# Kernel optimization log

Measured on AMD Instinct MI355X. Metric: run time of the kernel, lower is better.

The kernel has to match this reference:

```python
import jax, jax.numpy as jnp
import numpy as np

N_LAYER = 4; D_MODEL = 512; D_INNER = 1024; D_STATE = 16
DT_RANK = 32; D_CONV = 3; VOCAB = 128; SEQ = 1024; HID = 2048; BATCH = 4
EPS = 1e-5

def layernorm(x, w, b):
    m = jnp.mean(x, -1, keepdims=True)
    v = jnp.mean((x - m) ** 2, -1, keepdims=True)
    return (x - m) * jax.lax.rsqrt(v + EPS) * w + b

def rmsnorm(x, w):
    return x * jax.lax.rsqrt(jnp.mean(x * x, -1, keepdims=True) + EPS) * w

def selective_scan(u, delta, A, B, C, D):
    # u, delta: (b,l,d); B,C: (b,l,n); A: (d,n); D: (d,)
    def step(s, inp):
        d_t, B_t, C_t, u_t = inp  # (b,d),(b,n),(b,n),(b,d)
        dA = jnp.exp(d_t[..., None] * A)                    # (b,d,n)
        dBu = (d_t * u_t)[..., None] * B_t[:, None, :]      # (b,d,n)
        s = dA * s + dBu
        return s, jnp.einsum('bdn,bn->bd', s, C_t)
    b, l, d = u.shape
    s0 = jnp.zeros((b, d, A.shape[1]), u.dtype)
    xs = (delta.swapaxes(0, 1), B.swapaxes(0, 1), C.swapaxes(0, 1), u.swapaxes(0, 1))
    _, ys = jax.lax.scan(step, s0, xs)
    return ys.swapaxes(0, 1) + u * D

def mamba_block(x, ln_w, ln_b, W_in, cw, cb, W_x, W_dt, b_dt, A_log, Dp, W_out):
    # ResidualBlock in source is norm -> mixer with NO residual add
    x = layernorm(x, ln_w, ln_b)
    xr = x @ W_in                               # (b,l,2*d_inner)
    xs, res = jnp.split(xr, 2, axis=-1)
    # depthwise causal conv (torch pads d_conv-1 both sides then slices [:l] == left-pad only)
    xc = jax.lax.conv_general_dilated(
        xs.swapaxes(1, 2), cw[:, None, :], (1,), [(D_CONV - 1, 0)],
        feature_group_count=D_INNER, dimension_numbers=('NCH', 'OIH', 'NCH'))
    xc = jax.nn.silu((xc + cb[:, None]).swapaxes(1, 2))  # (b,l,d_inner)
    A = -jnp.exp(A_log)
    x_dbl = xc @ W_x
    delta, B, C = jnp.split(x_dbl, [DT_RANK, DT_RANK + D_STATE], axis=-1)
    delta = jax.nn.softplus(delta @ W_dt + b_dt)
    y = selective_scan(xc, delta, A, B, C, Dp)
    return (y * jax.nn.silu(res)) @ W_out

def reference(inp, W_emb, b_emb,
              ln1_w, ln1_b, Win1, cw1, cb1, Wx1, Wdt1, bdt1, Alog1, D1, Wout1,
              ln2_w, ln2_b, Win2, cw2, cb2, Wx2, Wdt2, bdt2, Alog2, D2, Wout2,
              lnl_w, lnl_b, Wl1, bl1, Wl2, bl2,
              normf_w, normf_b, W_head, b_head):
    x = inp @ W_emb + b_emb
    x1 = x; x2 = x
    for i in range(N_LAYER):
        x1 = mamba_block(x1, ln1_w[i], ln1_b[i], Win1[i], cw1[i], cb1[i],
                         Wx1[i], Wdt1[i], bdt1[i], Alog1[i], D1[i], Wout1[i])
        x2 = mamba_block(jnp.flip(x2, 1), ln2_w[i], ln2_b[i], Win2[i], cw2[i], cb2[i],
                         Wx2[i], Wdt2[i], bdt2[i], Alog2[i], D2[i], Wout2[i])
        x = x1 + jnp.flip(x2, 1) + x
        xp = x.swapaxes(1, 2)                   # (b, d_model, seq)
        h = layernorm(xp, lnl_w[i], lnl_b[i]) if i == 0 else rmsnorm(xp, lnl_w[i])
        h = jax.nn.relu(h @ Wl1[i] + bl1[i]) @ Wl2[i] + bl2[i]
        x = h.swapaxes(1, 2) + x
        x1 = x; x2 = x
    x = layernorm(x, normf_w, normf_b)
    return x @ W_head + b_head

def setup_inputs():
    key = jax.random.key(0)
    ks = iter(jax.random.split(key, 80))
    r = lambda shape, s=0.02: jax.random.normal(next(ks), shape, jnp.float32) * s
    L, D, DI, N, R, K, V, S, H = N_LAYER, D_MODEL, D_INNER, D_STATE, DT_RANK, D_CONV, VOCAB, SEQ, HID
    def dirp():
        return [jnp.ones((L, D)), jnp.zeros((L, D)), r((L, D, 2 * DI)),
                r((L, DI, K), 0.2), jnp.zeros((L, DI)), r((L, DI, R + 2 * N)),
                r((L, R, DI), 0.1), jnp.zeros((L, DI)),
                jnp.broadcast_to(jnp.log(jnp.arange(1.0, N + 1)), (L, DI, N)) + 0.0,
                jnp.ones((L, DI)), r((L, DI, D))]
    p1 = dirp(); p2 = dirp()
    d = {"inp": jax.random.normal(next(ks), (BATCH, S, V), jnp.float32),
         "W_emb": r((V, D)), "b_emb": jnp.zeros((D,))}
    n1 = ["ln1_w", "ln1_b", "Win1", "cw1", "cb1", "Wx1", "Wdt1", "bdt1", "Alog1", "D1", "Wout1"]
    n2 = ["ln2_w", "ln2_b", "Win2", "cw2", "cb2", "Wx2", "Wdt2", "bdt2", "Alog2", "D2", "Wout2"]
    d.update(dict(zip(n1, p1))); d.update(dict(zip(n2, p2)))
    d.update({"lnl_w": jnp.ones((L, S)), "lnl_b": jnp.zeros((L, S)),
              "Wl1": r((L, S, H)), "bl1": jnp.zeros((L, H)),
              "Wl2": r((L, H, S)), "bl2": jnp.zeros((L, S)),
              "normf_w": jnp.ones((D,)), "normf_b": jnp.zeros((D,)),
              "W_head": r((D, V)), "b_head": jnp.zeros((V,))})
    return d
```

## Files before the change

kernel.cpp:

```cpp
#include <hip/hip_runtime.h>
#include <math.h>

#define NLAYER 4
#define DM 512
#define DI 1024
#define NS 16
#define RK 32
#define VOC 128
#define S 1024
#define HD 2048
#define B 4
#define TOK (B*S)
#define TOK2 (2*TOK)
#define EPSF 1e-5f
#define NC 32
#define CL 32

typedef unsigned short u16;
typedef __attribute__((ext_vector_type(8))) short bf16x8;
typedef __attribute__((ext_vector_type(4))) float f32x4;

__device__ __forceinline__ float siluf(float x){ return x / (1.f + __expf(-x)); }
__device__ __forceinline__ float softplusf(float x){
    return x > 20.f ? x : __logf(1.f + __expf(x));
}
__device__ __forceinline__ u16 f2bf(float f){
    unsigned u = __float_as_uint(f);
    u += 0x7fffu + ((u >> 16) & 1u);
    return (u16)(u >> 16);
}
__device__ __forceinline__ float bf2f(u16 v){ return __uint_as_float(((unsigned)v) << 16); }

__device__ __forceinline__ void powchain16(float a1, float* e){
    float a2 = a1*a1, a4 = a2*a2, a8 = a4*a4;
    e[0]=a1;      e[1]=a2;      e[2]=a2*a1;   e[3]=a4;
    e[4]=a4*a1;   e[5]=a4*a2;   e[6]=a4*e[2]; e[7]=a8;
    e[8]=a8*a1;   e[9]=a8*a2;   e[10]=a8*e[2];e[11]=a8*a4;
    e[12]=a8*e[4];e[13]=a8*e[5];e[14]=a8*e[6];e[15]=a8*a8;
}

template<int BM, int ACT, bool BIAS, bool OUTBF16>
__launch_bounds__(256)
__global__ void mgemm_k(const u16* __restrict__ A,
                        const u16* __restrict__ Bt0, const u16* __restrict__ Bt1,
                        const float* __restrict__ bias0, const float* __restrict__ bias1,
                        void* __restrict__ Cv, int M, int N, int K, int Ksl, int mh,
                        size_t zstride)
{
    constexpr int LOGBM = (BM == 128) ? 7 : 6;
    constexpr int NI = (BM == 128) ? 4 : 2;
    constexpr int SSZ = BM*32 + 128*32;
    __shared__ u16 smem[3*SSZ];
    const int tid  = threadIdx.x;
    const int wave = tid >> 6;
    const int lane = tid & 63;
    const int nwg  = gridDim.x * gridDim.y;
    const int orig = blockIdx.y * gridDim.x + blockIdx.x;
    const int q = nwg >> 3, r = nwg & 7;
    const int xcd = orig & 7, sid = orig >> 3;
    const int nid = (xcd < r ? xcd*(q+1) : r*(q+1) + (xcd-r)*q) + sid;
    const int m_blk = (nid / gridDim.x) * BM;
    const int n_blk = (nid % gridDim.x) * 128;
    const int dir = (m_blk >= mh) ? 1 : 0;
    const u16* Bt = dir ? Bt1 : Bt0;
    const float* bias = dir ? bias1 : bias0;
    const int wm = (BM == 128) ? (wave & 1) * 64 : 0;
    const int wn = (BM == 128) ? (wave >> 1) * 64 : wave * 32;
    const int kbeg = blockIdx.z * Ksl;

    f32x4 acc[4][NI];
    #pragma unroll
    for (int i=0;i<4;i++)
        #pragma unroll
        for (int j=0;j<NI;j++){ f32x4 z = {0.f,0.f,0.f,0.f}; acc[i][j] = z; }

    const u16* Ag = A + (size_t)(m_blk + (tid & (BM-1))) * K + ((tid >> LOGBM) * 8) + kbeg;
    const u16* Bg = Bt + (size_t)(n_blk + (tid & 127)) * K + ((tid >> 7) * 8) + kbeg;
    const int la = lane & 15, ga = lane >> 4;

    auto stage = [&](int k0, int st){
        u16* Al = smem + st*SSZ;
        u16* Bl = Al + BM*32;
        #pragma unroll
        for (int c = 0; c < BM/64; ++c)
            __builtin_amdgcn_global_load_lds(
                (const __attribute__((address_space(1))) unsigned int*)(Ag + k0 + c*16),
                (__attribute__((address_space(3))) unsigned int*)&Al[(c*256 + tid)*8],
                16, 0, 0);
        #pragma unroll
        for (int c = 0; c < 2; ++c)
            __builtin_amdgcn_global_load_lds(
                (const __attribute__((address_space(1))) unsigned int*)(Bg + k0 + c*16),
                (__attribute__((address_space(3))) unsigned int*)&Bl[(c*256 + tid)*8],
                16, 0, 0);
    };

    const int niter = Ksl >> 5;
    stage(0, 0);
    stage(32, 1);
    for (int it = 0; it < niter; ++it) {
        if (it < niter-1) {
            if (BM == 128)
                asm volatile("s_waitcnt vmcnt(4) lgkmcnt(0)\n\ts_barrier" ::: "memory");
            else
                asm volatile("s_waitcnt vmcnt(3) lgkmcnt(0)\n\ts_barrier" ::: "memory");
        } else {
            asm volatile("s_waitcnt vmcnt(0) lgkmcnt(0)\n\ts_barrier" ::: "memory");
        }
        if (it + 2 < niter) stage((it+2)*32, (it+2)%3);
        const u16* Ab = smem + (it%3)*SSZ;
        const u16* Bb = Ab + BM*32;
        bf16x8 af[4], bf[NI];
        #pragma unroll
        for (int mi=0;mi<4;mi++)
            af[mi] = *(const bf16x8*)&Ab[((ga*BM) + wm + mi*16 + la)*8];
        #pragma unroll
        for (int ni=0;ni<NI;ni++)
            bf[ni] = *(const bf16x8*)&Bb[((ga*128) + wn + ni*16 + la)*8];
        #pragma unroll
        for (int mi=0;mi<4;mi++)
            #pragma unroll
            for (int ni=0;ni<NI;ni++)
                acc[mi][ni] = __builtin_amdgcn_mfma_f32_16x16x32_bf16(af[mi], bf[ni], acc[mi][ni], 0,0,0);
    }

    const int col = lane & 15;
    const int r4  = (lane >> 4) * 4;
    asm volatile("s_waitcnt lgkmcnt(0)\n\ts_barrier" ::: "memory");
    if (OUTBF16) {
        u16* Cs = smem;
        #pragma unroll
        for (int mi=0;mi<4;mi++){
            #pragma unroll
            for (int ni=0;ni<NI;ni++){
                int cc = wn + ni*16 + col;
                float bv = BIAS ? bias[n_blk + cc] : 0.f;
                #pragma unroll
                for (int r=0;r<4;r++){
                    float v = acc[mi][ni][r] + bv;
                    if (ACT==1) v = fmaxf(v, 0.f);
                    Cs[(wm + mi*16 + r4 + r)*128 + cc] = f2bf(v);
                }
            }
        }
        asm volatile("s_waitcnt lgkmcnt(0)\n\ts_barrier" ::: "memory");
        u16* Cg = (u16*)Cv + (size_t)blockIdx.z * zstride;
        #pragma unroll
        for (int k=0;k<BM/16;k++){
            int q2 = k*256 + tid;
            int row = q2 >> 4, co = (q2 & 15) * 8;
            uint4 v = *(const uint4*)&Cs[row*128 + co];
            *(uint4*)(Cg + (size_t)(m_blk+row)*N + n_blk + co) = v;
        }
    } else {
        float* Csf = (float*)smem;
        float* Cg = (float*)Cv + (size_t)blockIdx.z * zstride;
        #pragma unroll
        for (int h=0; h<2; ++h){
            if ((wn >> 6) == h){
                #pragma unroll
                for (int mi=0;mi<4;mi++){
                    #pragma unroll
                    for (int ni=0;ni<NI;ni++){
                        int cc = wn - h*64 + ni*16 + col;
                        float bv = BIAS ? bias[n_blk + h*64 + cc] : 0.f;
                        #pragma unroll
                        for (int r=0;r<4;r++){
                            float v = acc[mi][ni][r] + bv;
                            if (ACT==1) v = fmaxf(v, 0.f);
                            Csf[(mi*16 + r4 + r)*64 + cc] = v;
                        }
                    }
                }
            }
            asm volatile("s_waitcnt lgkmcnt(0)\n\ts_barrier" ::: "memory");
            #pragma unroll
            for (int k=0;k<4;k++){
                int q2 = k*256 + tid;
                int row = q2 >> 4, co = (q2 & 15) * 4;
                float4 v = *(const float4*)&Csf[row*64 + co];
                *(float4*)(Cg + (size_t)(m_blk+row)*N + n_blk + h*64 + co) = v;
            }
            if (h == 0)
                asm volatile("s_waitcnt lgkmcnt(0)\n\ts_barrier" ::: "memory");
        }
    }
}

__launch_bounds__(256)
__global__ void gemm_wx_k(const u16* __restrict__ A, const u16* __restrict__ Bt,
                          float* __restrict__ C, int K, int Ksl)
{
    constexpr int SSZ = 128*32 + 128*32;
    __shared__ u16 smem[3*SSZ];
    const int tid  = threadIdx.x;
    const int wave = tid >> 6;
    const int lane = tid & 63;
    const int m_blk = blockIdx.y * 128;
    const int dir = (m_blk >= TOK) ? 1 : 0;
    const int wm = (wave & 1) * 64;
    const int wn = (wave >> 1) * 64;
    const int kbeg = blockIdx.z * Ksl;

    f32x4 acc[4][4];
    #pragma unroll
    for (int i=0;i<4;i++)
        #pragma unroll
        for (int j=0;j<4;j++){ f32x4 z = {0.f,0.f,0.f,0.f}; acc[i][j] = z; }

    const u16* Ag = A + (size_t)(m_blk + (tid & 127)) * K + ((tid >> 7) * 8) + kbeg;
    const u16* Bg = Bt + (size_t)(tid & 127) * K + ((tid >> 7) * 8) + kbeg;
    const int la = lane & 15, ga = lane >> 4;

    auto stage = [&](int k0, int st){
        u16* Al = smem + st*SSZ;
        u16* Bl = Al + 128*32;
        #pragma unroll
        for (int c = 0; c < 2; ++c){
            __builtin_amdgcn_global_load_lds(
                (const __attribute__((address_space(1))) unsigned int*)(Ag + k0 + c*16),
                (__attribute__((address_space(3))) unsigned int*)&Al[(c*256 + tid)*8],
                16, 0, 0);
            __builtin_amdgcn_global_load_lds(
                (const __attribute__((address_space(1))) unsigned int*)(Bg + k0 + c*16),
                (__attribute__((address_space(3))) unsigned int*)&Bl[(c*256 + tid)*8],
                16, 0, 0);
        }
    };

    const int niter = Ksl >> 5;
    stage(0, 0);
    stage(32, 1);
    for (int it = 0; it < niter; ++it) {
        if (it < niter-1)
            asm volatile("s_waitcnt vmcnt(4) lgkmcnt(0)\n\ts_barrier" ::: "memory");
        else
            asm volatile("s_waitcnt vmcnt(0) lgkmcnt(0)\n\ts_barrier" ::: "memory");
        if (it + 2 < niter) stage((it+2)*32, (it+2)%3);
        const u16* Ab = smem + (it%3)*SSZ;
        const u16* Bb = Ab + 128*32;
        bf16x8 af[4], bf[4];
        #pragma unroll
        for (int mi=0;mi<4;mi++)
            af[mi] = *(const bf16x8*)&Ab[((ga*128) + wm + mi*16 + la)*8];
        #pragma unroll
        for (int ni=0;ni<4;ni++)
            bf[ni] = *(const bf16x8*)&Bb[((ga*128) + wn + ni*16 + la)*8];
        #pragma unroll
        for (int mi=0;mi<4;mi++)
            #pragma unroll
            for (int ni=0;ni<4;ni++)
                acc[mi][ni] = __builtin_amdgcn_mfma_f32_16x16x32_bf16(af[mi], bf[ni], acc[mi][ni], 0,0,0);
    }

    const int col = lane & 15;
    const int r4  = (lane >> 4) * 4;
    #pragma unroll
    for (int mi=0;mi<4;mi++){
        #pragma unroll
        for (int ni=0;ni<4;ni++){
            int cg = wn + ni*16 + col;
            if ((cg >> 6) != dir) continue;
            int co = cg & 63;
            #pragma unroll
            for (int r=0;r<4;r++){
                int rg = m_blk + wm + mi*16 + r4 + r;
                atomicAdd(C + (size_t)rg*64 + co, acc[mi][ni][r]);
            }
        }
    }
}

__global__ void wtconv2_k(const float* __restrict__ W0, const float* __restrict__ W1,
                          u16* __restrict__ T0, u16* __restrict__ T1, int K, int N)
{
    const float* W = blockIdx.z ? W1 : W0;
    u16* Wt = blockIdx.z ? T1 : T0;
    __shared__ float tile[32][33];
    int n0 = blockIdx.x*32, k0 = blockIdx.y*32;
    int tx = threadIdx.x, ty = threadIdx.y;
    #pragma unroll
    for (int j=0;j<32;j+=8)
        tile[ty+j][tx] = W[(size_t)(k0+ty+j)*N + n0+tx];
    __syncthreads();
    #pragma unroll
    for (int j=0;j<32;j+=8)
        Wt[(size_t)(n0+ty+j)*K + k0+tx] = f2bf(tile[tx][ty+j]);
}

template<int ACT, bool BIAS>
__launch_bounds__(256)
__global__ void gemm_k(const float* __restrict__ A, int lda,
                       const float* __restrict__ Bm, int ldb,
                       const float* __restrict__ bias,
                       float* __restrict__ C, int ldc, int K)
{
    __shared__ float As[16][64];
    __shared__ float Bs[16][64];
    const int tid = threadIdx.x;
    const int n0 = blockIdx.x * 64;
    const int m0 = blockIdx.y * 64;
    const int tn = (tid & 15) * 4;
    const int tm = (tid >> 4) * 4;
    const int am = tid >> 2;
    const int ak = (tid & 3) * 4;
    const int bk = tid >> 4;
    const int bn = (tid & 15) * 4;
    float acc[4][4] = {};
    for (int k0 = 0; k0 < K; k0 += 16) {
        float4 av = *(const float4*)(A + (size_t)(m0 + am) * lda + k0 + ak);
        float4 bv = *(const float4*)(Bm + (size_t)(k0 + bk) * ldb + n0 + bn);
        __syncthreads();
        As[ak+0][am] = av.x; As[ak+1][am] = av.y; As[ak+2][am] = av.z; As[ak+3][am] = av.w;
        *(float4*)(&Bs[bk][bn]) = bv;
        __syncthreads();
        #pragma unroll
        for (int k = 0; k < 16; ++k) {
            float4 a = *(const float4*)(&As[k][tm]);
            float4 b = *(const float4*)(&Bs[k][tn]);
            float aa[4] = {a.x,a.y,a.z,a.w};
            float bb[4] = {b.x,b.y,b.z,b.w};
            #pragma unroll
            for (int i=0;i<4;i++)
                #pragma unroll
                for (int j=0;j<4;j++)
                    acc[i][j] = fmaf(aa[i], bb[j], acc[i][j]);
        }
    }
    #pragma unroll
    for (int i=0;i<4;i++)
        #pragma unroll
        for (int j=0;j<4;j++){
            float v = acc[i][j];
            if (BIAS) v += bias[n0+tn+j];
            if (ACT==1) v = fmaxf(v, 0.f);
            C[(size_t)(m0+tm+i)*ldc + n0+tn+j] = v;
        }
}

__launch_bounds__(256)
__global__ void gemm_sk_k(const float* __restrict__ A, int lda,
                          const float* __restrict__ Bm, int ldb,
                          const float* __restrict__ bias,
                          float* __restrict__ C, int ldc, int kslice)
{
    __shared__ float As[16][64];
    __shared__ float Bs[16][64];
    const int tid = threadIdx.x;
    const int n0 = blockIdx.x * 64;
    const int m0 = blockIdx.y * 64;
    const int kbeg = blockIdx.z * kslice;
    const int tn = (tid & 15) * 4;
    const int tm = (tid >> 4) * 4;
    const int am = tid >> 2;
    const int ak = (tid & 3) * 4;
    const int bk = tid >> 4;
    const int bn = (tid & 15) * 4;
    float acc[4][4] = {};
    for (int k0 = kbeg; k0 < kbeg + kslice; k0 += 16) {
        float4 av = *(const float4*)(A + (size_t)(m0 + am) * lda + k0 + ak);
        float4 bv = *(const float4*)(Bm + (size_t)(k0 + bk) * ldb + n0 + bn);
        __syncthreads();
        As[ak+0][am] = av.x; As[ak+1][am] = av.y; As[ak+2][am] = av.z; As[ak+3][am] = av.w;
        *(float4*)(&Bs[bk][bn]) = bv;
        __syncthreads();
        #pragma unroll
        for (int k = 0; k < 16; ++k) {
            float4 a = *(const float4*)(&As[k][tm]);
            float4 b = *(const float4*)(&Bs[k][tn]);
            float aa[4] = {a.x,a.y,a.z,a.w};
            float bb[4] = {b.x,b.y,b.z,b.w};
            #pragma unroll
            for (int i=0;i<4;i++)
                #pragma unroll
                for (int j=0;j<4;j++)
                    acc[i][j] = fmaf(aa[i], bb[j], acc[i][j]);
        }
    }
    #pragma unroll
    for (int i=0;i<4;i++)
        #pragma unroll
        for (int j=0;j<4;j++){
            float v = acc[i][j];
            if (bias && blockIdx.z == 0) v += bias[n0+tn+j];
            atomicAdd(C + (size_t)(m0+tm+i)*ldc + n0+tn+j, v);
        }
}

__launch_bounds__(256)
__global__ void gemm_dt_k(const float* __restrict__ xdbl,
                          const float* __restrict__ Wdt0, const float* __restrict__ Wdt1,
                          const float* __restrict__ bdt0, const float* __restrict__ bdt1,
                          u16* __restrict__ delta)
{
    __shared__ float As[32][64];
    __shared__ float Bs[32][64];
    const int tid = threadIdx.x;
    const int n0 = blockIdx.x * 64;
    const int m0 = blockIdx.y * 64;
    const int dir = (m0 >= TOK) ? 1 : 0;
    const float* Wdt = dir ? Wdt1 : Wdt0;
    const float* bdt = dir ? bdt1 : bdt0;
    const int am = tid >> 2;
    const int ak = (tid & 3) * 8;
    {
        float4 a0 = *(const float4*)(xdbl + (size_t)(m0 + am) * 64 + ak);
        float4 a1 = *(const float4*)(xdbl + (size_t)(m0 + am) * 64 + ak + 4);
        As[ak+0][am]=a0.x; As[ak+1][am]=a0.y; As[ak+2][am]=a0.z; As[ak+3][am]=a0.w;
        As[ak+4][am]=a1.x; As[ak+5][am]=a1.y; As[ak+6][am]=a1.z; As[ak+7][am]=a1.w;
        int bk = tid >> 4;
        int bn = (tid & 15) * 4;
        *(float4*)(&Bs[bk][bn])    = *(const float4*)(Wdt + (size_t)bk*DI + n0 + bn);
        *(float4*)(&Bs[bk+16][bn]) = *(const float4*)(Wdt + (size_t)(bk+16)*DI + n0 + bn);
    }
    __syncthreads();
    const int tn = (tid & 15) * 4;
    const int tm = (tid >> 4) * 4;
    float acc[4][4] = {};
    #pragma unroll
    for (int k = 0; k < 32; ++k) {
        float4 a = *(const float4*)(&As[k][tm]);
        float4 b = *(const float4*)(&Bs[k][tn]);
        float aa[4] = {a.x,a.y,a.z,a.w};
        float bb[4] = {b.x,b.y,b.z,b.w};
        #pragma unroll
        for (int i=0;i<4;i++)
            #pragma unroll
            for (int j=0;j<4;j++)
                acc[i][j] = fmaf(aa[i], bb[j], acc[i][j]);
    }
    #pragma unroll
    for (int i=0;i<4;i++)
        #pragma unroll
        for (int j=0;j<4;j++)
            delta[(size_t)(m0+tm+i)*DI + n0+tn+j] = f2bf(softplusf(acc[i][j] + bdt[n0+tn+j]));
}

template<int LEN, bool RMS, bool OB>
__launch_bounds__(256)
__global__ void norm_k(const float* __restrict__ in, const float* __restrict__ w,
                       const float* __restrict__ b, void* __restrict__ outv)
{
    constexpr int PER = LEN/256;
    const int row = blockIdx.x;
    const float* x = in + (size_t)row * LEN;
    float v[PER];
    float s = 0.f, ss = 0.f;
    #pragma unroll
    for (int i=0;i<PER;i++){ v[i] = x[threadIdx.x + i*256]; s += v[i]; ss += v[i]*v[i]; }
    #pragma unroll
    for (int off=32; off; off>>=1){ s += __shfl_down(s, off); ss += __shfl_down(ss, off); }
    __shared__ float sh[8];
    int wid = threadIdx.x >> 6;
    if ((threadIdx.x & 63) == 0){ sh[wid] = s; sh[wid+4] = ss; }
    __syncthreads();
    s = sh[0]+sh[1]+sh[2]+sh[3]; ss = sh[4]+sh[5]+sh[6]+sh[7];
    float mean = RMS ? 0.f : s / (float)LEN;
    float var  = ss / (float)LEN - mean*mean;
    float r = rsqrtf(var + EPSF);
    #pragma unroll
    for (int i=0;i<PER;i++){
        int c = threadIdx.x + i*256;
        float y = (v[i]-mean)*r*w[c];
        if (!RMS) y += b[c];
        if (OB) ((u16*)outv)[(size_t)row*LEN + c] = f2bf(y);
        else    ((float*)outv)[(size_t)row*LEN + c] = y;
    }
}

__launch_bounds__(256)
__global__ void norm2_k(const float* __restrict__ in,
                        const float* __restrict__ w0, const float* __restrict__ b0,
                        const float* __restrict__ w1, const float* __restrict__ b1,
                        u16* __restrict__ outv)
{
    const int row = blockIdx.x;
    const int t = row & (TOK-1);
    const float* w = (row >= TOK) ? w1 : w0;
    const float* b = (row >= TOK) ? b1 : b0;
    const float* x = in + (size_t)t * DM;
    float v[2];
    float s = 0.f, ss = 0.f;
    #pragma unroll
    for (int i=0;i<2;i++){ v[i] = x[threadIdx.x + i*256]; s += v[i]; ss += v[i]*v[i]; }
    #pragma unroll
    for (int off=32; off; off>>=1){ s += __shfl_down(s, off); ss += __shfl_down(ss, off); }
    __shared__ float sh[8];
    int wid = threadIdx.x >> 6;
    if ((threadIdx.x & 63) == 0){ sh[wid] = s; sh[wid+4] = ss; }
    __syncthreads();
    s = sh[0]+sh[1]+sh[2]+sh[3]; ss = sh[4]+sh[5]+sh[6]+sh[7];
    float mean = s / (float)DM;
    float var  = ss / (float)DM - mean*mean;
    float r = rsqrtf(var + EPSF);
    #pragma unroll
    for (int i=0;i<2;i++){
        int c = threadIdx.x + i*256;
        outv[(size_t)row*DM + c] = f2bf((v[i]-mean)*r*w[c] + b[c]);
    }
}

__launch_bounds__(256)
__global__ void conv_silu2_k(const u16* __restrict__ xr,
                             const float* __restrict__ cw0, const float* __restrict__ cb0,
                             const float* __restrict__ cw1, const float* __restrict__ cb1,
                             u16* __restrict__ xcout)
{
    int idx = blockIdx.x*256 + threadIdx.x;
    int ch = idx & (DI-1);
    int row = idx >> 10;
    int l  = row & (S-1);
    int dir = row >> 12;
    int rev = dir;
    const float* cw = dir ? cw1 : cw0;
    const float* cb = dir ? cb1 : cb0;
    float acc = cb[ch];
    #pragma unroll
    for (int k=0;k<3;k++){
        int lp = rev ? (l + 2 - k) : (l - 2 + k);
        if (lp >= 0 && lp < S)
            acc = fmaf(cw[ch*3+k], bf2f(xr[(size_t)(row - l + lp)*2048 + ch]), acc);
    }
    xcout[(size_t)row*DI + ch] = f2bf(siluf(acc));
}

__launch_bounds__(256)
__global__ void add3_k(const float* __restrict__ xin, const float* __restrict__ yw,
                       float* __restrict__ acc)
{
    int i = (blockIdx.x*256 + threadIdx.x)*4;
    float4 a = *(const float4*)(xin + i);
    float4 b = *(const float4*)(yw + i);
    float4 c = *(const float4*)(yw + (size_t)TOK*DM + i);
    float4 o = {a.x+b.x+c.x, a.y+b.y+c.y, a.z+b.z+c.z, a.w+b.w+c.w};
    *(float4*)(acc + i) = o;
}

__launch_bounds__(256)
__global__ void scan_part1_k(const u16* __restrict__ xc, const u16* __restrict__ delta,
                             const float* __restrict__ xdbl,
                             const float* __restrict__ Alog0, const float* __restrict__ Alog1,
                             float* __restrict__ sumP, float* __restrict__ sumS)
{
    const int g = blockIdx.x;
    const int chg = g & 3;
    const int c   = (g >> 2) & (NC-1);
    const int db  = g >> 7;
    const int dir = db >> 2;
    const int rev = dir;
    const int tid = threadIdx.x;
    const int ch  = chg*256 + tid;

    __shared__ float Bsh[CL][16];
    #pragma unroll
    for (int r=0;r<2;r++){
        int idx = r*256 + tid;
        int j = idx >> 4, w = idx & 15;
        int p = c*CL + j;
        int t = rev ? (S-1-p) : p;
        Bsh[j][w] = xdbl[((size_t)(db*S + t))*64 + 32 + w];
    }
    __syncthreads();

    const float* Alog = dir ? Alog1 : Alog0;
    const float An0 = -__expf(Alog[(size_t)ch*16]);

    float s[16];
    #pragma unroll
    for (int n=0;n<16;n++) s[n] = 0.f;
    float dsum = 0.f;
    for (int j=0;j<CL;j++){
        int p = c*CL + j;
        int t = rev ? (S-1-p) : p;
        size_t tt = (size_t)(db*S + t);
        float dl = bf2f(delta[tt*DI + ch]);
        float ul = bf2f(xc[tt*DI + ch]);
        dsum += dl;
        float dlu = dl*ul;
        float Bv[16];
        *(float4*)&Bv[0]  = *(const float4*)&Bsh[j][0];
        *(float4*)&Bv[4]  = *(const float4*)&Bsh[j][4];
        *(float4*)&Bv[8]  = *(const float4*)&Bsh[j][8];
        *(float4*)&Bv[12] = *(const float4*)&Bsh[j][12];
        float e[16];
        powchain16(__expf(dl*An0), e);
        #pragma unroll
        for (int n=0;n<16;n++)
            s[n] = fmaf(e[n], s[n], dlu*Bv[n]);
    }
    size_t base = ((size_t)(db*NC + c)*DI + ch)*16;
    float P[16];
    powchain16(__expf(dsum*An0), P);
    #pragma unroll
    for (int q=0;q<4;q++){
        *(float4*)(sumP + base + q*4) = *(float4*)&P[q*4];
        *(float4*)(sumS + base + q*4) = *(float4*)&s[q*4];
    }
}

__launch_bounds__(256)
__global__ void scan_part2_k(float* __restrict__ sumP, const float* __restrict__ sumS)
{
    int g = blockIdx.x*256 + threadIdx.x;
    int idx = g & (DI*16 - 1);
    int db = g >> 14;
    float carry = 0.f;
    #pragma unroll 8
    for (int c=0;c<NC;c++){
        size_t o = (size_t)(db*NC + c)*DI*16 + idx;
        float P = sumP[o], Sv = sumS[o];
        sumP[o] = carry;
        carry = fmaf(P, carry, Sv);
    }
}

__launch_bounds__(256)
__global__ void scan_part3_k(const u16* __restrict__ xc, const u16* __restrict__ delta,
                             const float* __restrict__ xdbl,
                             const float* __restrict__ Alog0, const float* __restrict__ Alog1,
                             const float* __restrict__ Dp0, const float* __restrict__ Dp1,
                             const u16* __restrict__ xr, const float* __restrict__ sumI,
                             u16* __restrict__ ybb)
{
    const int g = blockIdx.x;
    const int chg = g & 3;
    const int c   = (g >> 2) & (NC-1);
    const int db  = g >> 7;
    const int dir = db >> 2;
    const int rev = dir;
    const int tid = threadIdx.x;
    const int ch  = chg*256 + tid;

    __shared__ float BC[CL][32];
    #pragma unroll
    for (int r=0;r<4;r++){
        int idx = r*256 + tid;
        int j = idx >> 5, w = idx & 31;
        int p = c*CL + j;
        int t = rev ? (S-1-p) : p;
        BC[j][w] = xdbl[((size_t)(db*S + t))*64 + 32 + w];
    }
    __syncthreads();

    const float* Alog = dir ? Alog1 : Alog0;
    const float An0 = -__expf(Alog[(size_t)ch*16]);
    const float dch = (dir ? Dp1 : Dp0)[ch];

    float s[16];
    size_t base = ((size_t)(db*NC + c)*DI + ch)*16;
    #pragma unroll
    for (int q=0;q<4;q++){
        float4 iv = *(const float4*)(sumI + base + q*4);
        s[q*4+0]=iv.x; s[q*4+1]=iv.y; s[q*4+2]=iv.z; s[q*4+3]=iv.w;
    }
    for (int j=0;j<CL;j++){
        int p = c*CL + j;
        int t = rev ? (S-1-p) : p;
        size_t tt = (size_t)(db*S + t);
        float dl = bf2f(delta[tt*DI + ch]);
        float ul = bf2f(xc[tt*DI + ch]);
        float res = bf2f(xr[tt*2048 + 1024 + ch]);
        float dlu = dl*ul;
        float Bv[16], Cv[16];
        *(float4*)&Bv[0]  = *(const float4*)&BC[j][0];
        *(float4*)&Bv[4]  = *(const float4*)&BC[j][4];
        *(float4*)&Bv[8]  = *(const float4*)&BC[j][8];
        *(float4*)&Bv[12] = *(const float4*)&BC[j][12];
        *(float4*)&Cv[0]  = *(const float4*)&BC[j][16];
        *(float4*)&Cv[4]  = *(const float4*)&BC[j][20];
        *(float4*)&Cv[8]  = *(const float4*)&BC[j][24];
        *(float4*)&Cv[12] = *(const float4*)&BC[j][28];
        float e[16];
        powchain16(__expf(dl*An0), e);
        float y = 0.f;
        #pragma unroll
        for (int n=0;n<16;n++){
            s[n] = fmaf(e[n], s[n], dlu*Bv[n]);
            y = fmaf(s[n], Cv[n], y);
        }
        y = (y + ul*dch) * siluf(res);
        ybb[tt*DI + ch] = f2bf(y);
    }
}

__global__ void transpose_k(const float* __restrict__ in, float* __restrict__ out)
{
    __shared__ float tile[32][33];
    int b = blockIdx.z, s0 = blockIdx.x*32, d0 = blockIdx.y*32;
    int tx = threadIdx.x, ty = threadIdx.y;
    #pragma unroll
    for (int j=0;j<32;j+=8)
        tile[ty+j][tx] = in[((size_t)b*S + s0+ty+j)*DM + d0+tx];
    __syncthreads();
    #pragma unroll
    for (int j=0;j<32;j+=8)
        out[((size_t)b*DM + d0+ty+j)*S + s0+tx] = tile[tx][ty+j];
}
__global__ void transpose_add_k(const float* __restrict__ h, const float* __restrict__ bias,
                                float* __restrict__ x)
{
    __shared__ float tile[32][33];
    int b = blockIdx.z, s0 = blockIdx.x*32, d0 = blockIdx.y*32;
    int tx = threadIdx.x, ty = threadIdx.y;
    #pragma unroll
    for (int j=0;j<32;j+=8){
        size_t o = ((size_t)b*DM + d0+ty+j)*S + s0+tx;
        tile[ty+j][tx] = h[o] + h[o + (size_t)2048*1024];
    }
    __syncthreads();
    #pragma unroll
    for (int j=0;j<32;j+=8)
        x[((size_t)b*S + s0+ty+j)*DM + d0+tx] += tile[tx][ty+j] + bias[s0+ty+j];
}

extern "C" void kernel_launch(void* const* d_in, const int* in_sizes, int n_in,
                              void* d_out, int out_size, void* d_ws, size_t ws_size,
                              hipStream_t stream)
{
    (void)in_sizes; (void)n_in; (void)out_size; (void)ws_size;
    const float* inp    = (const float*)d_in[0];
    const float* W_emb  = (const float*)d_in[1];
    const float* b_emb  = (const float*)d_in[2];
    const float* lnw_[2]  = {(const float*)d_in[3],  (const float*)d_in[14]};
    const float* lnb_[2]  = {(const float*)d_in[4],  (const float*)d_in[15]};
    const float* Win_[2]  = {(const float*)d_in[5],  (const float*)d_in[16]};
    const float* cw_[2]   = {(const float*)d_in[6],  (const float*)d_in[17]};
    const float* cb_[2]   = {(const float*)d_in[7],  (const float*)d_in[18]};
    const float* Wx_[2]   = {(const float*)d_in[8],  (const float*)d_in[19]};
    const float* Wdt_[2]  = {(const float*)d_in[9],  (const float*)d_in[20]};
    const float* bdt_[2]  = {(const float*)d_in[10], (const float*)d_in[21]};
    const float* Alog_[2] = {(const float*)d_in[11], (const float*)d_in[22]};
    const float* Dp_[2]   = {(const float*)d_in[12], (const float*)d_in[23]};
    const float* Wout_[2] = {(const float*)d_in[13], (const float*)d_in[24]};
    const float* lnl_w  = (const float*)d_in[25];
    const float* lnl_b  = (const float*)d_in[26];
    const float* Wl1    = (const float*)d_in[27];
    const float* bl1    = (const float*)d_in[28];
    const float* Wl2    = (const float*)d_in[29];
    const float* bl2    = (const float*)d_in[30];
    const float* normf_w= (const float*)d_in[31];
    const float* normf_b= (const float*)d_in[32];
    const float* W_head = (const float*)d_in[33];
    const float* b_head = (const float*)d_in[34];
    float* out = (float*)d_out;

    float* ws = (float*)d_ws;
    size_t off = 0;
    auto alloc = [&](size_t n){ float* p = ws + off; off += n; return p; };
    const size_t M1 = 1024*1024;
    float* Xa    = alloc(2*M1);
    float* Xb    = alloc(2*M1);
    float* XR2f  = alloc(8*M1);
    float* XC2f  = alloc(4*M1);
    float* XDBL2 = alloc(M1/2);
    float* DELTA2= alloc(4*M1);
    float* Ybb2f = alloc(2*M1);
    float* XLN2f = alloc(2*M1);
    float* WinT2f= alloc(1*M1);
    float* WoutT2f = alloc(M1/2);
    float* WxT2f = alloc(M1/16);
    float* sumP  = alloc(4*M1);
    float* sumS  = alloc(4*M1);

    u16* XR2   = (u16*)XR2f;
    u16* XC2   = (u16*)XC2f;
    u16* DELTA2b = (u16*)DELTA2;
    u16* Ybb2  = (u16*)Ybb2f;
    u16* XLN2  = (u16*)XLN2f;
    u16* WinT0 = (u16*)WinT2f;             u16* WinT1 = WinT0 + 2048*512;
    u16* WoutT0= (u16*)WoutT2f;            u16* WoutT1= WoutT0 + 512*1024;
    u16* WxT   = (u16*)WxT2f;
    float* YW  = sumS;
    u16*  H1b  = (u16*)XR2f;
    u16*  Wl1T = (u16*)(XR2f + 2*M1);
    u16*  Wl2T = (u16*)(XR2f + 3*M1);
    float* H2  = XR2f + 4*M1;
    float* XP  = XC2f;
    float* XF  = XC2f;

    gemm_k<0,true><<<dim3(DM/64, TOK/64), 256, 0, stream>>>(
        inp, VOC, W_emb, DM, b_emb, Xa, DM, VOC);

    float* xin = Xa;
    float* acc = Xb;
    for (int i = 0; i < NLAYER; ++i) {
        wtconv2_k<<<dim3(2048/32, DM/32, 2), dim3(32,8), 0, stream>>>(
            Win_[0]+(size_t)i*DM*2048, Win_[1]+(size_t)i*DM*2048, WinT0, WinT1, DM, 2048);
        wtconv2_k<<<dim3(DM/32, DI/32, 2), dim3(32,8), 0, stream>>>(
            Wout_[0]+(size_t)i*DI*DM, Wout_[1]+(size_t)i*DI*DM, WoutT0, WoutT1, DI, DM);
        wtconv2_k<<<dim3(64/32, DI/32, 2), dim3(32,8), 0, stream>>>(
            Wx_[0]+(size_t)i*DI*64, Wx_[1]+(size_t)i*DI*64, WxT, WxT + 64*DI, DI, 64);
        norm2_k<<<TOK2, 256, 0, stream>>>(
            xin, lnw_[0]+i*DM, lnb_[0]+i*DM, lnw_[1]+i*DM, lnb_[1]+i*DM, XLN2);
        mgemm_k<128,0,false,true><<<dim3(2048/128, TOK2/128), 256, 0, stream>>>(
            XLN2, WinT0, WinT1, nullptr, nullptr, XR2, TOK2, 2048, DM, DM, TOK, 0);
        conv_silu2_k<<<TOK2*DI/256, 256, 0, stream>>>(
            XR2, cw_[0]+(size_t)i*DI*3, cb_[0]+(size_t)i*DI,
            cw_[1]+(size_t)i*DI*3, cb_[1]+(size_t)i*DI, XC2);
        hipMemsetAsync(XDBL2, 0, (size_t)TOK2*64*sizeof(float), stream);
        gemm_wx_k<<<dim3(1, TOK2/128, 4), 256, 0, stream>>>(
            XC2, WxT, XDBL2, DI, DI/4);
        gemm_dt_k<<<dim3(DI/64, TOK2/64), 256, 0, stream>>>(
            XDBL2, Wdt_[0]+(size_t)i*RK*DI, Wdt_[1]+(size_t)i*RK*DI,
            bdt_[0]+(size_t)i*DI, bdt_[1]+(size_t)i*DI, DELTA2b);
        scan_part1_k<<<8*NC*4, 256, 0, stream>>>(
            XC2, DELTA2b, XDBL2,
            Alog_[0]+(size_t)i*DI*NS, Alog_[1]+(size_t)i*DI*NS, sumP, sumS);
        scan_part2_k<<<8*DI*16/256, 256, 0, stream>>>(sumP, sumS);
        scan_part3_k<<<8*NC*4, 256, 0, stream>>>(
            XC2, DELTA2b, XDBL2,
            Alog_[0]+(size_t)i*DI*NS, Alog_[1]+(size_t)i*DI*NS,
            Dp_[0]+(size_t)i*DI, Dp_[1]+(size_t)i*DI, XR2, sumP, Ybb2);
        mgemm_k<64,0,false,false><<<dim3(DM/128, TOK2/64), 256, 0, stream>>>(
            Ybb2, WoutT0, WoutT1, nullptr, nullptr, YW, TOK2, DM, DI, DI, TOK, 0);
        add3_k<<<TOK*DM/1024, 256, 0, stream>>>(xin, YW, acc);
        transpose_k<<<dim3(S/32, DM/32, B), dim3(32,8), 0, stream>>>(acc, XP);
        if (i == 0)
            norm_k<S,false,true><<<B*DM, 256, 0, stream>>>(XP, lnl_w, lnl_b, XLN2);
        else
            norm_k<S,true ,true><<<B*DM, 256, 0, stream>>>(XP, lnl_w+(size_t)i*S, nullptr, XLN2);
        wtconv2_k<<<dim3(HD/32, S/32, 1), dim3(32,8), 0, stream>>>(
            Wl1+(size_t)i*S*HD, nullptr, Wl1T, nullptr, S, HD);
        wtconv2_k<<<dim3(S/32, HD/32, 1), dim3(32,8), 0, stream>>>(
            Wl2+(size_t)i*HD*S, nullptr, Wl2T, nullptr, HD, S);
        mgemm_k<64,1,true,true><<<dim3(HD/128, (B*DM)/64), 256, 0, stream>>>(
            XLN2, Wl1T, Wl1T, bl1+(size_t)i*HD, bl1+(size_t)i*HD, H1b,
            B*DM, HD, S, S, 1<<30, 0);
        mgemm_k<64,0,false,false><<<dim3(S/128, (B*DM)/64, 2), 256, 0, stream>>>(
            H1b, Wl2T, Wl2T, nullptr, nullptr, H2, B*DM, S, HD, HD/2, 1<<30,
            (size_t)2048*1024);
        transpose_add_k<<<dim3(S/32, DM/32, B), dim3(32,8), 0, stream>>>(
            H2, bl2+(size_t)i*S, acc);
        float* tmp = xin; xin = acc; acc = tmp;
    }

    norm_k<DM,false,false><<<TOK, 256, 0, stream>>>(xin, normf_w, normf_b, XF);
    hipMemsetAsync(out, 0, (size_t)TOK*VOC*sizeof(float), stream);
    gemm_sk_k<<<dim3(VOC/64, TOK/64, 4), 256, 0, stream>>>(
        XF, DM, W_head, VOC, b_head, out, VOC, 128);
}
```

Measured before the change: 1.348 ms.

## Add 256x128 tile in-projection GEMM with XCD swizzle and vectorize conv-silu

Replaces the in-projection GEMM with a new 512-thread kernel using 256x128 output tiles, a triple-buffered global-to-LDS load pipeline, and XCD-aware block remapping so neighbouring tiles share an L2. This is meant to raise data reuse and MFMA utilization in the largest per-layer GEMM. Separately, the depthwise conv+silu kernel now handles 8 channels per thread with 16-byte loads and stores instead of one scalar element each, cutting memory instruction count. The larger tile and 512-thread block raise register and LDS pressure and reduce the number of blocks in the grid.

```diff
diff --git a/kernel.cpp b/kernel.cpp
--- a/kernel.cpp
+++ b/kernel.cpp
@@ -187,6 +187,101 @@
     }
 }
 
+__launch_bounds__(512, 4)
+__global__ void mgemm256_k(const u16* __restrict__ A,
+                           const u16* __restrict__ Bt0, const u16* __restrict__ Bt1,
+                           u16* __restrict__ C, int N, int K, int mh)
+{
+    constexpr int SSZ = 256*32 + 128*32;
+    __shared__ u16 smem[3*SSZ];
+    const int tid  = threadIdx.x;
+    const int wave = tid >> 6;
+    const int lane = tid & 63;
+    const int nwg  = gridDim.x * gridDim.y;
+    const int orig = blockIdx.y * gridDim.x + blockIdx.x;
+    const int q = nwg >> 3;
+    const int xcd = orig & 7, sid = orig >> 3;
+    const int nid = xcd*q + sid;
+    const int m_blk = (nid / gridDim.x) * 256;
+    const int n_blk = (nid % gridDim.x) * 128;
+    const u16* Bt = (m_blk >= mh) ? Bt1 : Bt0;
+    const int wm = (wave >> 1) * 64;
+    const int wn = (wave & 1) * 64;
+
+    f32x4 acc[4][4];
+    #pragma unroll
+    for (int i=0;i<4;i++)
+        #pragma unroll
+        for (int j=0;j<4;j++){ f32x4 z = {0.f,0.f,0.f,0.f}; acc[i][j] = z; }
+
+    const u16* Ag = A + (size_t)(m_blk + (tid & 255)) * K + ((tid >> 8) * 8);
+    const u16* Bg = Bt + (size_t)(n_blk + (tid & 127)) * K + ((tid >> 7) * 8);
+    const int la = lane & 15, ga = lane >> 4;
+
+    auto stage = [&](int k0, int st){
+        u16* Al = smem + st*SSZ;
+        u16* Bl = Al + 256*32;
+        #pragma unroll
+        for (int c = 0; c < 2; ++c)
+            __builtin_amdgcn_global_load_lds(
+                (const __attribute__((address_space(1))) unsigned int*)(Ag + k0 + c*16),
+                (__attribute__((address_space(3))) unsigned int*)&Al[(c*512 + tid)*8],
+                16, 0, 0);
+        __builtin_amdgcn_global_load_lds(
+            (const __attribute__((address_space(1))) unsigned int*)(Bg + k0),
+            (__attribute__((address_space(3))) unsigned int*)&Bl[tid*8],
+            16, 0, 0);
+    };
+
+    const int niter = K >> 5;
+    stage(0, 0);
+    stage(32, 1);
+    for (int it = 0; it < niter; ++it) {
+        if (it < niter-1)
+            asm volatile("s_waitcnt vmcnt(3) lgkmcnt(0)\n\ts_barrier" ::: "memory");
+        else
+            asm volatile("s_waitcnt vmcnt(0) lgkmcnt(0)\n\ts_barrier" ::: "memory");
+        if (it + 2 < niter) stage((it+2)*32, (it+2)%3);
+        const u16* Ab = smem + (it%3)*SSZ;
+        const u16* Bb = Ab + 256*32;
+        bf16x8 af[4], bf[4];
+        #pragma unroll
+        for (int mi=0;mi<4;mi++)
+            af[mi] = *(const bf16x8*)&Ab[((ga*256) + wm + mi*16 + la)*8];
+        #pragma unroll
+        for (int ni=0;ni<4;ni++)
+            bf[ni] = *(const bf16x8*)&Bb[((ga*128) + wn + ni*16 + la)*8];
+        #pragma unroll
+        for (int mi=0;mi<4;mi++)
+            #pragma unroll
+            for (int ni=0;ni<4;ni++)
+                acc[mi][ni] = __builtin_amdgcn_mfma_f32_16x16x32_bf16(af[mi], bf[ni], acc[mi][ni], 0,0,0);
+    }
+
+    const int col = lane & 15;
+    const int r4  = (lane >> 4) * 4;
+    asm volatile("s_waitcnt lgkmcnt(0)\n\ts_barrier" ::: "memory");
+    u16* Cs = smem;
+    #pragma unroll
+    for (int mi=0;mi<4;mi++){
+        #pragma unroll
+        for (int ni=0;ni<4;ni++){
+            int cc = wn + ni*16 + col;
+            #pragma unroll
+            for (int r=0;r<4;r++)
+                Cs[(wm + mi*16 + r4 + r)*128 + cc] = f2bf(acc[mi][ni][r]);
+        }
+    }
+    asm volatile("s_waitcnt lgkmcnt(0)\n\ts_barrier" ::: "memory");
+    #pragma unroll
+    for (int k=0;k<8;k++){
+        int q2 = k*512 + tid;
+        int row = q2 >> 4, co = (q2 & 15) * 8;
+        uint4 v = *(const uint4*)&Cs[row*128 + co];
+        *(uint4*)(C + (size_t)(m_blk+row)*N + n_blk + co) = v;
+    }
+}
+
 __launch_bounds__(256)
 __global__ void gemm_wx_k(const u16* __restrict__ A, const u16* __restrict__ Bt,
                           float* __restrict__ C, int K, int Ksl)
@@ -507,21 +602,29 @@
                              u16* __restrict__ xcout)
 {
     int idx = blockIdx.x*256 + threadIdx.x;
-    int ch = idx & (DI-1);
-    int row = idx >> 10;
+    int c0 = (idx & 127) * 8;
+    int row = idx >> 7;
     int l  = row & (S-1);
     int dir = row >> 12;
-    int rev = dir;
     const float* cw = dir ? cw1 : cw0;
     const float* cb = dir ? cb1 : cb0;
-    float acc = cb[ch];
+    float a[8];
+    #pragma unroll
+    for (int j=0;j<8;j++) a[j] = cb[c0+j];
     #pragma unroll
     for (int k=0;k<3;k++){
-        int lp = rev ? (l + 2 - k) : (l - 2 + k);
-        if (lp >= 0 && lp < S)
-            acc = fmaf(cw[ch*3+k], bf2f(xr[(size_t)(row - l + lp)*2048 + ch]), acc);
-    }
-    xcout[(size_t)row*DI + ch] = f2bf(siluf(acc));
+        int lp = dir ? (l + 2 - k) : (l - 2 + k);
+        if (lp >= 0 && lp < S){
+            bf16x8 v = *(const bf16x8*)&xr[(size_t)(row - l + lp)*2048 + c0];
+            #pragma unroll
+            for (int j=0;j<8;j++)
+                a[j] = fmaf(cw[(c0+j)*3+k], bf2f((u16)v[j]), a[j]);
+        }
+    }
+    bf16x8 o;
+    #pragma unroll
+    for (int j=0;j<8;j++) o[j] = (short)f2bf(siluf(a[j]));
+    *(bf16x8*)&xcout[(size_t)row*DI + c0] = o;
 }
 
 __launch_bounds__(256)
@@ -792,9 +895,9 @@
             Wx_[0]+(size_t)i*DI*64, Wx_[1]+(size_t)i*DI*64, WxT, WxT + 64*DI, DI, 64);
         norm2_k<<<TOK2, 256, 0, stream>>>(
             xin, lnw_[0]+i*DM, lnb_[0]+i*DM, lnw_[1]+i*DM, lnb_[1]+i*DM, XLN2);
-        mgemm_k<128,0,false,true><<<dim3(2048/128, TOK2/128), 256, 0, stream>>>(
-            XLN2, WinT0, WinT1, nullptr, nullptr, XR2, TOK2, 2048, DM, DM, TOK, 0);
-        conv_silu2_k<<<TOK2*DI/256, 256, 0, stream>>>(
+        mgemm256_k<<<dim3(2048/128, TOK2/256), 512, 0, stream>>>(
+            XLN2, WinT0, WinT1, XR2, 2048, DM, TOK);
+        conv_silu2_k<<<TOK2*DI/8/256, 256, 0, stream>>>(
             XR2, cw_[0]+(size_t)i*DI*3, cb_[0]+(size_t)i*DI,
             cw_[1]+(size_t)i*DI*3, cb_[1]+(size_t)i*DI, XC2);
         hipMemsetAsync(XDBL2, 0, (size_t)TOK2*64*sizeof(float), stream);
```

Measured after the change: 1.460 ms. +8.3%, slower.
